# Kernel optimization log

Hardware: AMD Instinct MI355X
Metric: run time of the kernel (lower is better)

Reference implementation:

```python
import jax, jax.numpy as jnp
import numpy as np

N = 50000      # nodes
E = 800000     # edges (avg degree 16)
F_IN = 512
HID = 128
OUT = 40


def setup_inputs() -> dict:
    key = jax.random.key(0)
    ks = jax.random.split(key, 6)
    x = jax.random.normal(ks[0], (N, F_IN), dtype=jnp.float32)
    edge_index = jax.random.randint(ks[1], (2, E), 0, N, dtype=jnp.int64)
    edge_weight = jax.random.uniform(ks[2], (E,), dtype=jnp.float32)
    # Glorot-ish init for the two GCNConv weight matrices
    W1 = jax.random.normal(ks[3], (F_IN, HID), dtype=jnp.float32) * (1.0 / np.sqrt(F_IN))
    b1 = jnp.zeros((HID,), dtype=jnp.float32)
    W2 = jax.random.normal(ks[4], (HID, OUT), dtype=jnp.float32) * (1.0 / np.sqrt(HID))
    b2 = jnp.zeros((OUT,), dtype=jnp.float32)
    return {"x": x, "edge_index": edge_index, "edge_weight": edge_weight,
            "W1": W1, "b1": b1, "W2": W2, "b2": b2}


def gcn_layer(x, edge_index, edge_weight, W, b):
    """PyG GCNConv (normalize=True, add_self_loops=True):
    out = D^{-1/2} (A + I) D^{-1/2} (x @ W) + b, with weighted edges."""
    n = x.shape[0]
    h = x @ W  # [n, F_out] dense transform before aggregation
    sl = jnp.arange(n)
    row = jnp.concatenate([edge_index[0], sl])   # source nodes
    col = jnp.concatenate([edge_index[1], sl])   # target nodes
    w = jnp.concatenate([edge_weight, jnp.ones((n,), x.dtype)])  # self-loop weight 1
    deg = jax.ops.segment_sum(w, col, num_segments=n)            # in-degree (weighted)
    dinv = jnp.where(deg > 0, jax.lax.rsqrt(deg), 0.0)
    norm = dinv[row] * w * dinv[col]                             # per-edge coefficient
    # gather-source, scale, scatter-add into target
    out = jax.ops.segment_sum(h[row] * norm[:, None], col, num_segments=n)
    return out + b


def reference(x, edge_index, edge_weight, W1, b1, W2, b2):
    h = jax.nn.relu(gcn_layer(x, edge_index, edge_weight, W1, b1))
    # dropout is identity at inference (training=False)
    h = gcn_layer(h, edge_index, edge_weight, W2, b2)
    return jax.nn.log_softmax(h, axis=1)
```

## Files before the change

### kernel.cpp

```cpp
#include <hip/hip_runtime.h>
#include <math.h>

#define N_NODES 50000
#define F_IN    512
#define HID     128
#define OUT_C   40
#define NPAD    48
#define E_EDGES 800000
#define SCAN_BLOCKS 196
#define LDA 40
#define LDK 136
#define MAXDEG 96
#define G1B 391
#define DEGB 3125

typedef __attribute__((ext_vector_type(8))) short short8;
typedef __attribute__((ext_vector_type(4))) float f32x4;

__device__ __forceinline__ unsigned short f2bf(float f) {
    union { float f; unsigned u; } v; v.f = f;
    unsigned u = v.u + 0x7fffu + ((v.u >> 16) & 1u);
    return (unsigned short)(u >> 16);
}
__device__ __forceinline__ float bf2f(unsigned short h) {
    return __uint_as_float((unsigned)h << 16);
}


__global__ void k_init(unsigned long long* __restrict__ packed) {
    int i = blockIdx.x * blockDim.x + threadIdx.x;
    if (i < N_NODES) packed[i] = 0ULL;
}


__global__ __launch_bounds__(256) void k_wprep(const float* __restrict__ W1,
                                               const float* __restrict__ W2,
                                               unsigned short* __restrict__ W1bt,
                                               unsigned short* __restrict__ W2bt) {
    int idx = blockIdx.x * 256 + threadIdx.x;
    if (idx < F_IN * HID) {
        int k = idx & 511, n = idx >> 9;
        W1bt[(size_t)n * F_IN + k] = f2bf(W1[(size_t)k * HID + n]);
    } else if (idx < F_IN * HID + NPAD * HID) {
        int i2 = idx - F_IN * HID;
        int k = i2 & 127, n = i2 >> 7;
        W2bt[n * HID + k] = (n < OUT_C) ? f2bf(W2[(size_t)k * OUT_C + n]) : 0;
    }
}


__global__ __launch_bounds__(256) void k_g1deg(const float* __restrict__ X,
                                               const unsigned short* __restrict__ W1bt,
                                               unsigned short* __restrict__ Hb,
                                               const int* __restrict__ col,
                                               const float* __restrict__ ew,
                                               unsigned long long* __restrict__ packed,
                                               int* __restrict__ rank) {
    const int tid = threadIdx.x;
    if (blockIdx.x >= G1B) {
        int e = (blockIdx.x - G1B) * 256 + tid;
        if (e < E_EDGES) {
            int c = col[e];
            unsigned long long fx = (unsigned long long)(ew[e] * 4294967296.0f);
            unsigned long long old = atomicAdd(&packed[c], (1ULL << 40) | fx);
            rank[e] = (int)(old >> 40);
        }
        return;
    }

    __shared__ __align__(16) unsigned short As[128 * LDA];
    __shared__ __align__(16) unsigned short Bs[128 * LDA];
    const int row0 = blockIdx.x * 128;
    const int lane = tid & 63;
    const int w    = tid >> 6;
    const int quad = lane >> 4;
    const int l16  = lane & 15;
    const int wm   = (w >> 1) * 64;
    const int wn   = (w & 1) * 64;

    f32x4 acc[4][4] = {};

    const int sr = tid >> 1;
    const int kg = (tid & 1) * 16;
    int arow = row0 + sr;
    if (arow >= N_NODES) arow = N_NODES - 1;
    const float*          xp = X + (size_t)arow * F_IN + kg;
    const unsigned short* bp = W1bt + (size_t)sr * F_IN + kg;
    unsigned short* asw = &As[sr * LDA + kg];
    unsigned short* bsw = &Bs[sr * LDA + kg];

    for (int k0 = 0; k0 < F_IN; k0 += 32) {
        float4 xa = *(const float4*)(xp + k0);
        float4 xb = *(const float4*)(xp + k0 + 4);
        float4 xc = *(const float4*)(xp + k0 + 8);
        float4 xd = *(const float4*)(xp + k0 + 12);
        short8 pa, pb;
        pa[0] = (short)f2bf(xa.x); pa[1] = (short)f2bf(xa.y);
        pa[2] = (short)f2bf(xa.z); pa[3] = (short)f2bf(xa.w);
        pa[4] = (short)f2bf(xb.x); pa[5] = (short)f2bf(xb.y);
        pa[6] = (short)f2bf(xb.z); pa[7] = (short)f2bf(xb.w);
        pb[0] = (short)f2bf(xc.x); pb[1] = (short)f2bf(xc.y);
        pb[2] = (short)f2bf(xc.z); pb[3] = (short)f2bf(xc.w);
        pb[4] = (short)f2bf(xd.x); pb[5] = (short)f2bf(xd.y);
        pb[6] = (short)f2bf(xd.z); pb[7] = (short)f2bf(xd.w);
        short8 wa = *(const short8*)(bp + k0);
        short8 wb = *(const short8*)(bp + k0 + 8);

        *(short8*)(asw)     = pa;
        *(short8*)(asw + 8) = pb;
        *(short8*)(bsw)     = wa;
        *(short8*)(bsw + 8) = wb;
        __syncthreads();

        short8 af[4], bf[4];
#pragma unroll
        for (int i = 0; i < 4; i++)
            af[i] = *(const short8*)&As[(wm + i * 16 + l16) * LDA + quad * 8];
#pragma unroll
        for (int j = 0; j < 4; j++)
            bf[j] = *(const short8*)&Bs[(wn + j * 16 + l16) * LDA + quad * 8];
#pragma unroll
        for (int i = 0; i < 4; i++)
#pragma unroll
            for (int j = 0; j < 4; j++)
                acc[i][j] = __builtin_amdgcn_mfma_f32_16x16x32_bf16(
                    af[i], bf[j], acc[i][j], 0, 0, 0);
        __syncthreads();
    }

#pragma unroll
    for (int i = 0; i < 4; i++) {
#pragma unroll
        for (int r = 0; r < 4; r++) {
            int grow = row0 + wm + i * 16 + quad * 4 + r;
            if (grow < N_NODES) {
#pragma unroll
                for (int j = 0; j < 4; j++) {
                    int gcol = wn + j * 16 + l16;
                    Hb[(size_t)grow * HID + gcol] = f2bf(acc[i][j][r]);
                }
            }
        }
    }
}


__global__ __launch_bounds__(256) void k_scan1(const unsigned long long* __restrict__ packed,
                                               int* __restrict__ excl,
                                               int* __restrict__ bsum,
                                               float* __restrict__ dinv) {
    __shared__ int s[256];
    int tid = threadIdx.x;
    int i = blockIdx.x * 256 + tid;
    unsigned long long pk = (i < N_NODES) ? packed[i] : 0ULL;
    int v = (int)(pk >> 40);
    if (i < N_NODES) {
        float d = 1.0f + (float)(pk & 0xFFFFFFFFFFULL) * (1.0f / 4294967296.0f);
        dinv[i] = rsqrtf(d);
    }
    s[tid] = v;
    __syncthreads();
#pragma unroll
    for (int off = 1; off < 256; off <<= 1) {
        int t = (tid >= off) ? s[tid - off] : 0;
        __syncthreads();
        s[tid] += t;
        __syncthreads();
    }
    if (i < N_NODES) excl[i] = s[tid] - v;
    if (tid == 255) bsum[blockIdx.x] = s[255];
}

__global__ __launch_bounds__(256) void k_scan2(int* __restrict__ bsum) {
    __shared__ int s[256];
    int tid = threadIdx.x;
    int v = (tid < SCAN_BLOCKS) ? bsum[tid] : 0;
    s[tid] = v;
    __syncthreads();
#pragma unroll
    for (int off = 1; off < 256; off <<= 1) {
        int t = (tid >= off) ? s[tid - off] : 0;
        __syncthreads();
        s[tid] += t;
        __syncthreads();
    }
    if (tid < SCAN_BLOCKS) bsum[tid] = s[tid] - v;
}

__global__ __launch_bounds__(256) void k_scan3(int* __restrict__ rowptr,
                                               const int* __restrict__ bsum) {
    int i = blockIdx.x * 256 + threadIdx.x;
    if (i < N_NODES) rowptr[i] += bsum[blockIdx.x];
    if (i == 0) rowptr[N_NODES] = E_EDGES;
}


__global__ void k_scatter(const int* __restrict__ row, const int* __restrict__ col,
                          const float* __restrict__ w, const float* __restrict__ dinv,
                          const int* __restrict__ rowptr, const int* __restrict__ rank,
                          int2* __restrict__ es) {
    int e = blockIdx.x * blockDim.x + threadIdx.x;
    if (e < E_EDGES) {
        int r = row[e], c = col[e];
        float pre = dinv[r] * w[e];
        int pos = rowptr[c] + rank[e];
        es[pos] = make_int2(r, __float_as_int(pre));
    }
}


__global__ __launch_bounds__(256) void k_agg1_csr(const int* __restrict__ rowptr,
                                                  const int2* __restrict__ es,
                                                  const float* __restrict__ dinv,
                                                  const unsigned short* __restrict__ H1b,
                                                  const float* __restrict__ b1,
                                                  unsigned short* __restrict__ A1b) {
    __shared__ int2 sE[4][MAXDEG];
    const int tid  = threadIdx.x;
    const int wv   = tid >> 6;
    const int lane = tid & 63;
    const int node = blockIdx.x * 4 + wv;
    if (node >= N_NODES) return;

    const int beg = rowptr[node];
    const int d   = rowptr[node + 1] - beg;
    const int dl  = (d < MAXDEG) ? d : MAXDEG;
    const int dp  = (dl + 7) & ~7;
    for (int p = lane; p < dp; p += 64)
        sE[wv][p] = (p < dl) ? es[beg + p] : make_int2(0, 0);

    const float di = dinv[node];
    const unsigned self = *(const unsigned*)&H1b[(size_t)node * HID + lane * 2];
    float al0 = di * __uint_as_float(self << 16);
    float ah0 = di * __uint_as_float(self & 0xffff0000u);
    float al1 = 0.0f, ah1 = 0.0f, al2 = 0.0f, ah2 = 0.0f, al3 = 0.0f, ah3 = 0.0f;

    for (int p = 0; p < dp; p += 8) {
        int s[8]; float n[8]; unsigned g[8];
#pragma unroll
        for (int j = 0; j < 8; j++) {
            int2 t = sE[wv][p + j];
            s[j] = t.x; n[j] = __int_as_float(t.y);
        }
#pragma unroll
        for (int j = 0; j < 8; j++)
            g[j] = *(const unsigned*)&H1b[(size_t)s[j] * HID + lane * 2];
        al0 = fmaf(__uint_as_float(g[0] << 16), n[0], al0);
        ah0 = fmaf(__uint_as_float(g[0] & 0xffff0000u), n[0], ah0);
        al1 = fmaf(__uint_as_float(g[1] << 16), n[1], al1);
        ah1 = fmaf(__uint_as_float(g[1] & 0xffff0000u), n[1], ah1);
        al2 = fmaf(__uint_as_float(g[2] << 16), n[2], al2);
        ah2 = fmaf(__uint_as_float(g[2] & 0xffff0000u), n[2], ah2);
        al3 = fmaf(__uint_as_float(g[3] << 16), n[3], al3);
        ah3 = fmaf(__uint_as_float(g[3] & 0xffff0000u), n[3], ah3);
        al0 = fmaf(__uint_as_float(g[4] << 16), n[4], al0);
        ah0 = fmaf(__uint_as_float(g[4] & 0xffff0000u), n[4], ah0);
        al1 = fmaf(__uint_as_float(g[5] << 16), n[5], al1);
        ah1 = fmaf(__uint_as_float(g[5] & 0xffff0000u), n[5], ah1);
        al2 = fmaf(__uint_as_float(g[6] << 16), n[6], al2);
        ah2 = fmaf(__uint_as_float(g[6] & 0xffff0000u), n[6], ah2);
        al3 = fmaf(__uint_as_float(g[7] << 16), n[7], al3);
        ah3 = fmaf(__uint_as_float(g[7] & 0xffff0000u), n[7], ah3);
    }
    for (int q = dl; q < d; ++q) {
        int2 t = es[beg + q];
        unsigned g = *(const unsigned*)&H1b[(size_t)t.x * HID + lane * 2];
        float nm = __int_as_float(t.y);
        al0 = fmaf(__uint_as_float(g << 16), nm, al0);
        ah0 = fmaf(__uint_as_float(g & 0xffff0000u), nm, ah0);
    }

    const float accl = (al0 + al1) + (al2 + al3);
    const float acch = (ah0 + ah1) + (ah2 + ah3);
    const int c = lane * 2;
    float rx = fmaxf(fmaf(di, accl, b1[c]), 0.0f);
    float ry = fmaxf(fmaf(di, acch, b1[c + 1]), 0.0f);
    unsigned pack = (unsigned)f2bf(rx) | ((unsigned)f2bf(ry) << 16);
    *(unsigned*)&A1b[(size_t)node * HID + c] = pack;
}


__global__ __launch_bounds__(256) void k_gemm2_mfma(const unsigned short* __restrict__ A1b,
                                                    const unsigned short* __restrict__ W2bt,
                                                    unsigned short* __restrict__ H2b) {
    __shared__ __align__(16) unsigned short As[128 * LDK];
    __shared__ __align__(16) unsigned short Bs[NPAD * LDK];
    const int tid  = threadIdx.x;
    const int row0 = blockIdx.x * 128;
    const int lane = tid & 63;
    const int w    = tid >> 6;
    const int quad = lane >> 4;
    const int l16  = lane & 15;

#pragma unroll
    for (int i = 0; i < 8; i++) {
        int id = tid + i * 256;
        int r = id >> 4, kc = (id & 15) * 8;
        int ar = row0 + r; if (ar >= N_NODES) ar = N_NODES - 1;
        *(short8*)&As[r * LDK + kc] = *(const short8*)&A1b[(size_t)ar * HID + kc];
    }
#pragma unroll
    for (int i = 0; i < 3; i++) {
        int id = tid + i * 256;
        int n = id >> 4, kc = (id & 15) * 8;
        *(short8*)&Bs[n * LDK + kc] = *(const short8*)&W2bt[n * HID + kc];
    }
    __syncthreads();

    f32x4 acc[2][3] = {};
    const int rbase = w * 32;
#pragma unroll
    for (int ks = 0; ks < 4; ks++) {
        const int k0 = ks * 32 + quad * 8;
        short8 af[2], bf[3];
#pragma unroll
        for (int i = 0; i < 2; i++)
            af[i] = *(const short8*)&As[(rbase + i * 16 + l16) * LDK + k0];
#pragma unroll
        for (int j = 0; j < 3; j++)
            bf[j] = *(const short8*)&Bs[(j * 16 + l16) * LDK + k0];
#pragma unroll
        for (int i = 0; i < 2; i++)
#pragma unroll
            for (int j = 0; j < 3; j++)
                acc[i][j] = __builtin_amdgcn_mfma_f32_16x16x32_bf16(
                    af[i], bf[j], acc[i][j], 0, 0, 0);
    }

#pragma unroll
    for (int i = 0; i < 2; i++) {
#pragma unroll
        for (int r = 0; r < 4; r++) {
            int grow = row0 + rbase + i * 16 + quad * 4 + r;
            if (grow < N_NODES) {
#pragma unroll
                for (int j = 0; j < 3; j++)
                    H2b[(size_t)grow * NPAD + j * 16 + l16] = f2bf(acc[i][j][r]);
            }
        }
    }
}


__global__ __launch_bounds__(256) void k_agg2_lsm(const int* __restrict__ rowptr,
                                                  const int2* __restrict__ es,
                                                  const float* __restrict__ dinv,
                                                  const unsigned short* __restrict__ H2b,
                                                  const float* __restrict__ b2,
                                                  float* __restrict__ out) {
    __shared__ int2 sE[4][MAXDEG];
    const int tid  = threadIdx.x;
    const int wv   = tid >> 6;
    const int lane = tid & 63;
    const int node = blockIdx.x * 4 + wv;
    if (node >= N_NODES) return;

    const int beg = rowptr[node];
    const int d   = rowptr[node + 1] - beg;
    const int dl = (d < MAXDEG) ? d : MAXDEG;
    const int dp = (dl + 7) & ~7;
    for (int p = lane; p < dp; p += 64)
        sE[wv][p] = (p < dl) ? es[beg + p] : make_int2(0, 0);

    float di = dinv[node];
    float a0 = 0.0f, a1 = 0.0f, a2 = 0.0f, a3 = 0.0f;
    if (lane < OUT_C) a0 = di * bf2f(H2b[(size_t)node * NPAD + lane]);

    for (int p = 0; p < dp; p += 8) {
        int s[8]; float n[8], v[8];
#pragma unroll
        for (int j = 0; j < 8; j++) {
            int2 t = sE[wv][p + j];
            s[j] = t.x; n[j] = __int_as_float(t.y);
        }
#pragma unroll
        for (int j = 0; j < 8; j++)
            v[j] = (lane < OUT_C) ? bf2f(H2b[(size_t)s[j] * NPAD + lane]) : 0.0f;
        a0 = fmaf(v[0], n[0], a0);  a1 = fmaf(v[1], n[1], a1);
        a2 = fmaf(v[2], n[2], a2);  a3 = fmaf(v[3], n[3], a3);
        a0 = fmaf(v[4], n[4], a0);  a1 = fmaf(v[5], n[5], a1);
        a2 = fmaf(v[6], n[6], a2);  a3 = fmaf(v[7], n[7], a3);
    }
    for (int q = dl; q < d; ++q)
        if (lane < OUT_C) {
            int2 t = es[beg + q];
            a0 = fmaf(bf2f(H2b[(size_t)t.x * NPAD + lane]), __int_as_float(t.y), a0);
        }

    float acc = (a0 + a1) + (a2 + a3);
    float v = (lane < OUT_C) ? fmaf(di, acc, b2[lane]) : -INFINITY;

    float m = v;
#pragma unroll
    for (int off = 32; off > 0; off >>= 1) m = fmaxf(m, __shfl_xor(m, off));
    float ex = (lane < OUT_C) ? __expf(v - m) : 0.0f;
    float s = ex;
#pragma unroll
    for (int off = 32; off > 0; off >>= 1) s += __shfl_xor(s, off);
    if (lane < OUT_C) out[(size_t)node * OUT_C + lane] = v - m - __logf(s);
}


extern "C" void kernel_launch(void* const* d_in, const int* in_sizes, int n_in,
                              void* d_out, int out_size, void* d_ws, size_t ws_size,
                              hipStream_t stream) {
    const float* x  = (const float*)d_in[0];
    const int*   ei = (const int*)d_in[1];
    const float* ew = (const float*)d_in[2];
    const float* W1 = (const float*)d_in[3];
    const float* b1 = (const float*)d_in[4];
    const float* W2 = (const float*)d_in[5];
    const float* b2 = (const float*)d_in[6];
    float* out = (float*)d_out;

    const int* row = ei;
    const int* col = ei + E_EDGES;

    float* ws = (float*)d_ws;
    unsigned long long* packed = (unsigned long long*)ws;
    float* dinv   = ws + 100000;
    int*   rowptr = (int*)(ws + 150000);
    int*   bsum   = (int*)(ws + 200016);
    int2*  es     = (int2*)(ws + 200272);
    int*   rank   = (int*)(ws + 1800272);
    unsigned short* H1b  = (unsigned short*)(ws + 2600272);
    unsigned short* A1b  = (unsigned short*)(ws + 5800272);
    unsigned short* W1bt = (unsigned short*)(ws + 9000272);
    unsigned short* W2bt = (unsigned short*)(ws + 9033040);
    unsigned short* H2b  = (unsigned short*)(ws + 9036112);

    const int B = 256;

    k_init<<<(N_NODES + B - 1) / B, B, 0, stream>>>(packed);
    k_wprep<<<(F_IN * HID + NPAD * HID + B - 1) / B, B, 0, stream>>>(W1, W2, W1bt, W2bt);

    k_g1deg<<<G1B + DEGB, B, 0, stream>>>(x, W1bt, H1b, col, ew, packed, rank);

    k_scan1<<<SCAN_BLOCKS, B, 0, stream>>>(packed, rowptr, bsum, dinv);
    k_scan2<<<1, B, 0, stream>>>(bsum);
    k_scan3<<<SCAN_BLOCKS, B, 0, stream>>>(rowptr, bsum);

    k_scatter<<<(E_EDGES + B - 1) / B, B, 0, stream>>>(row, col, ew, dinv,
                                                       rowptr, rank, es);

    k_agg1_csr<<<(N_NODES + 3) / 4, B, 0, stream>>>(rowptr, es, dinv, H1b, b1, A1b);

    k_gemm2_mfma<<<(N_NODES + 127) / 128, B, 0, stream>>>(A1b, W2bt, H2b);

    k_agg2_lsm<<<(N_NODES + 3) / 4, B, 0, stream>>>(rowptr, es, dinv, H2b, b2, out);
}
```

Baseline: 310.0 us.

## Replace global-atomic degree counting with LDS chunked histograms for CSR build

Degree and rank computation moves from 64-bit global atomics per edge to per-block LDS histograms over 32 edge chunks × 4 node ranges. The per-chunk partial counts are scanned into absolute per-chunk offsets. A new scatter kernel recomputes local ranks with LDS atomics, so the rank array and the init kernel are no longer needed. Edge weights are now summed as 10-bit fixed point, which reduces degree precision. Only 128 blocks handle the histogram and scatter work, each rereading col, and the scans now read and write a 6.4MB partial array.

```diff
diff --git a/kernel.cpp b/kernel.cpp
--- a/kernel.cpp
+++ b/kernel.cpp
@@ -12,7 +12,10 @@
 #define LDK 136
 #define MAXDEG 96
 #define G1B 391
-#define DEGB 3125
+#define NCHUNK 32
+#define NRANGE 4
+#define RNODES 12500
+#define CHUNK_E 25000
 
 typedef __attribute__((ext_vector_type(8))) short short8;
 typedef __attribute__((ext_vector_type(4))) float f32x4;
@@ -24,12 +27,6 @@
 }
 __device__ __forceinline__ float bf2f(unsigned short h) {
     return __uint_as_float((unsigned)h << 16);
-}
-
-
-__global__ void k_init(unsigned long long* __restrict__ packed) {
-    int i = blockIdx.x * blockDim.x + threadIdx.x;
-    if (i < N_NODES) packed[i] = 0ULL;
 }
 
 
@@ -49,27 +46,39 @@
 }
 
 
-__global__ __launch_bounds__(256) void k_g1deg(const float* __restrict__ X,
-                                               const unsigned short* __restrict__ W1bt,
-                                               unsigned short* __restrict__ Hb,
-                                               const int* __restrict__ col,
-                                               const float* __restrict__ ew,
-                                               unsigned long long* __restrict__ packed,
-                                               int* __restrict__ rank) {
+__global__ __launch_bounds__(256) void k_g1hist(const float* __restrict__ X,
+                                                const unsigned short* __restrict__ W1bt,
+                                                unsigned short* __restrict__ Hb,
+                                                const int* __restrict__ col,
+                                                const float* __restrict__ ew,
+                                                unsigned* __restrict__ partial) {
+    __shared__ __align__(16) unsigned smem[12544];
     const int tid = threadIdx.x;
+
     if (blockIdx.x >= G1B) {
-        int e = (blockIdx.x - G1B) * 256 + tid;
-        if (e < E_EDGES) {
-            int c = col[e];
-            unsigned long long fx = (unsigned long long)(ew[e] * 4294967296.0f);
-            unsigned long long old = atomicAdd(&packed[c], (1ULL << 40) | fx);
-            rank[e] = (int)(old >> 40);
-        }
+        const int hb = blockIdx.x - G1B;
+        const int nc = hb >> 2, nr = hb & 3;
+        const int nbase = nr * RNODES;
+        unsigned* cnt = smem;
+        for (int i = tid; i < RNODES; i += 256) cnt[i] = 0u;
+        __syncthreads();
+        const int e0 = nc * CHUNK_E;
+        for (int k = tid; k < CHUNK_E; k += 256) {
+            int e = e0 + k;
+            unsigned cr = (unsigned)(col[e] - nbase);
+            if (cr < (unsigned)RNODES) {
+                unsigned fx = (unsigned)(ew[e] * 1024.0f + 0.5f);
+                atomicAdd(&cnt[cr], (1u << 16) | fx);
+            }
+        }
+        __syncthreads();
+        for (int i = tid; i < RNODES; i += 256)
+            partial[(size_t)nc * N_NODES + nbase + i] = cnt[i];
         return;
     }
 
-    __shared__ __align__(16) unsigned short As[128 * LDA];
-    __shared__ __align__(16) unsigned short Bs[128 * LDA];
+    unsigned short* As = (unsigned short*)smem;
+    unsigned short* Bs = As + 128 * LDA;
     const int row0 = blockIdx.x * 128;
     const int lane = tid & 63;
     const int w    = tid >> 6;
@@ -145,18 +154,26 @@
 }
 
 
-__global__ __launch_bounds__(256) void k_scan1(const unsigned long long* __restrict__ packed,
+__global__ __launch_bounds__(256) void k_scan1(unsigned* __restrict__ partial,
                                                int* __restrict__ excl,
                                                int* __restrict__ bsum,
                                                float* __restrict__ dinv) {
     __shared__ int s[256];
     int tid = threadIdx.x;
     int i = blockIdx.x * 256 + tid;
-    unsigned long long pk = (i < N_NODES) ? packed[i] : 0ULL;
-    int v = (int)(pk >> 40);
+    int v = 0;
     if (i < N_NODES) {
-        float d = 1.0f + (float)(pk & 0xFFFFFFFFFFULL) * (1.0f / 4294967296.0f);
-        dinv[i] = rsqrtf(d);
+        unsigned ctot = 0; float wsum = 0.0f;
+#pragma unroll
+        for (int nc = 0; nc < NCHUNK; nc++) {
+            size_t idx = (size_t)nc * N_NODES + i;
+            unsigned p = partial[idx];
+            partial[idx] = ctot;
+            ctot += p >> 16;
+            wsum += (float)(p & 0xffffu);
+        }
+        dinv[i] = rsqrtf(1.0f + wsum * (1.0f / 1024.0f));
+        v = (int)ctot;
     }
     s[tid] = v;
     __syncthreads();
@@ -187,24 +204,46 @@
     if (tid < SCAN_BLOCKS) bsum[tid] = s[tid] - v;
 }
 
+
 __global__ __launch_bounds__(256) void k_scan3(int* __restrict__ rowptr,
-                                               const int* __restrict__ bsum) {
+                                               const int* __restrict__ bsum,
+                                               unsigned* __restrict__ partial) {
     int i = blockIdx.x * 256 + threadIdx.x;
-    if (i < N_NODES) rowptr[i] += bsum[blockIdx.x];
+    if (i < N_NODES) {
+        int rp = rowptr[i] + bsum[blockIdx.x];
+        rowptr[i] = rp;
+#pragma unroll
+        for (int nc = 0; nc < NCHUNK; nc++)
+            partial[(size_t)nc * N_NODES + i] += (unsigned)rp;
+    }
     if (i == 0) rowptr[N_NODES] = E_EDGES;
 }
 
 
-__global__ void k_scatter(const int* __restrict__ row, const int* __restrict__ col,
-                          const float* __restrict__ w, const float* __restrict__ dinv,
-                          const int* __restrict__ rowptr, const int* __restrict__ rank,
-                          int2* __restrict__ es) {
-    int e = blockIdx.x * blockDim.x + threadIdx.x;
-    if (e < E_EDGES) {
-        int r = row[e], c = col[e];
-        float pre = dinv[r] * w[e];
-        int pos = rowptr[c] + rank[e];
-        es[pos] = make_int2(r, __float_as_int(pre));
+__global__ __launch_bounds__(256) void k_scatter2(const int* __restrict__ row,
+                                                  const int* __restrict__ col,
+                                                  const float* __restrict__ ew,
+                                                  const float* __restrict__ dinv,
+                                                  const unsigned* __restrict__ cbabs,
+                                                  int2* __restrict__ es) {
+    __shared__ unsigned cnt[RNODES];
+    const int tid = threadIdx.x;
+    const int nc = blockIdx.x >> 2, nr = blockIdx.x & 3;
+    const int nbase = nr * RNODES;
+    for (int i = tid; i < RNODES; i += 256) cnt[i] = 0u;
+    __syncthreads();
+    const int e0 = nc * CHUNK_E;
+    for (int k = tid; k < CHUNK_E; k += 256) {
+        int e = e0 + k;
+        int c = col[e];
+        unsigned cr = (unsigned)(c - nbase);
+        if (cr < (unsigned)RNODES) {
+            unsigned local = atomicAdd(&cnt[cr], 1u);
+            unsigned pos = cbabs[(size_t)nc * N_NODES + c] + local;
+            int r = row[e];
+            float pre = dinv[r] * ew[e];
+            es[pos] = make_int2(r, __float_as_int(pre));
+        }
     }
 }
 
@@ -417,31 +456,28 @@
     const int* col = ei + E_EDGES;
 
     float* ws = (float*)d_ws;
-    unsigned long long* packed = (unsigned long long*)ws;
-    float* dinv   = ws + 100000;
-    int*   rowptr = (int*)(ws + 150000);
-    int*   bsum   = (int*)(ws + 200016);
-    int2*  es     = (int2*)(ws + 200272);
-    int*   rank   = (int*)(ws + 1800272);
-    unsigned short* H1b  = (unsigned short*)(ws + 2600272);
-    unsigned short* A1b  = (unsigned short*)(ws + 5800272);
-    unsigned short* W1bt = (unsigned short*)(ws + 9000272);
-    unsigned short* W2bt = (unsigned short*)(ws + 9033040);
-    unsigned short* H2b  = (unsigned short*)(ws + 9036112);
+    unsigned* partial = (unsigned*)ws;
+    float* dinv   = ws + 1600000;
+    int*   rowptr = (int*)(ws + 1650016);
+    int*   bsum   = (int*)(ws + 1700032);
+    int2*  es     = (int2*)(ws + 1700352);
+    unsigned short* H1b  = (unsigned short*)(ws + 3300352);
+    unsigned short* A1b  = (unsigned short*)(ws + 6500352);
+    unsigned short* W1bt = (unsigned short*)(ws + 9700352);
+    unsigned short* W2bt = (unsigned short*)(ws + 9733120);
+    unsigned short* H2b  = (unsigned short*)(ws + 9736192);
 
     const int B = 256;
 
-    k_init<<<(N_NODES + B - 1) / B, B, 0, stream>>>(packed);
     k_wprep<<<(F_IN * HID + NPAD * HID + B - 1) / B, B, 0, stream>>>(W1, W2, W1bt, W2bt);
 
-    k_g1deg<<<G1B + DEGB, B, 0, stream>>>(x, W1bt, H1b, col, ew, packed, rank);
-
-    k_scan1<<<SCAN_BLOCKS, B, 0, stream>>>(packed, rowptr, bsum, dinv);
+    k_g1hist<<<G1B + NCHUNK * NRANGE, B, 0, stream>>>(x, W1bt, H1b, col, ew, partial);
+
+    k_scan1<<<SCAN_BLOCKS, B, 0, stream>>>(partial, rowptr, bsum, dinv);
     k_scan2<<<1, B, 0, stream>>>(bsum);
-    k_scan3<<<SCAN_BLOCKS, B, 0, stream>>>(rowptr, bsum);
-
-    k_scatter<<<(E_EDGES + B - 1) / B, B, 0, stream>>>(row, col, ew, dinv,
-                                                       rowptr, rank, es);
+    k_scan3<<<SCAN_BLOCKS, B, 0, stream>>>(rowptr, bsum, partial);
+
+    k_scatter2<<<NCHUNK * NRANGE, B, 0, stream>>>(row, col, ew, dinv, partial, es);
 
     k_agg1_csr<<<(N_NODES + 3) / 4, B, 0, stream>>>(rowptr, es, dinv, H1b, b1, A1b);
 
```

After: 428.4 us. 1.38x slower.

## Fuse init into wprep, merge scan stages, batch edges per thread, nontemporal loads

Applied to the files above, without the earlier changes.

Zeroing of the packed degree array moves into the weight-prep kernel, and the single-block scan2 is folded into scan3, where every block redundantly rescans the block sums. Together these remove two kernel launches. The degree-counting and scatter kernels now handle four edges per thread with fewer blocks, issuing the atomics before storing ranks. Nontemporal loads are used for X in the GEMM and for the edge arrays. The aim is less launch overhead and better memory-level parallelism, at the cost of redundant scan work in every block.

```diff
diff --git a/kernel.cpp b/kernel.cpp
--- a/kernel.cpp
+++ b/kernel.cpp
@@ -12,7 +12,8 @@
 #define LDK 136
 #define MAXDEG 96
 #define G1B 391
-#define DEGB 3125
+#define DEGB 782
+#define SCATB 782
 
 typedef __attribute__((ext_vector_type(8))) short short8;
 typedef __attribute__((ext_vector_type(4))) float f32x4;
@@ -27,16 +28,11 @@
 }
 
 
-__global__ void k_init(unsigned long long* __restrict__ packed) {
-    int i = blockIdx.x * blockDim.x + threadIdx.x;
-    if (i < N_NODES) packed[i] = 0ULL;
-}
-
-
 __global__ __launch_bounds__(256) void k_wprep(const float* __restrict__ W1,
                                                const float* __restrict__ W2,
                                                unsigned short* __restrict__ W1bt,
-                                               unsigned short* __restrict__ W2bt) {
+                                               unsigned short* __restrict__ W2bt,
+                                               unsigned long long* __restrict__ packed) {
     int idx = blockIdx.x * 256 + threadIdx.x;
     if (idx < F_IN * HID) {
         int k = idx & 511, n = idx >> 9;
@@ -45,6 +41,9 @@
         int i2 = idx - F_IN * HID;
         int k = i2 & 127, n = i2 >> 7;
         W2bt[n * HID + k] = (n < OUT_C) ? f2bf(W2[(size_t)k * OUT_C + n]) : 0;
+    } else {
+        int i3 = idx - (F_IN * HID + NPAD * HID);
+        if (i3 < N_NODES) packed[i3] = 0ULL;
     }
 }
 
@@ -58,12 +57,22 @@
                                                int* __restrict__ rank) {
     const int tid = threadIdx.x;
     if (blockIdx.x >= G1B) {
-        int e = (blockIdx.x - G1B) * 256 + tid;
-        if (e < E_EDGES) {
-            int c = col[e];
-            unsigned long long fx = (unsigned long long)(ew[e] * 4294967296.0f);
-            unsigned long long old = atomicAdd(&packed[c], (1ULL << 40) | fx);
-            rank[e] = (int)(old >> 40);
+        const int e0 = (blockIdx.x - G1B) * 1024 + tid;
+        unsigned long long old[4];
+#pragma unroll
+        for (int j = 0; j < 4; j++) {
+            int e = e0 + j * 256;
+            if (e < E_EDGES) {
+                int c = __builtin_nontemporal_load(col + e);
+                float w = __builtin_nontemporal_load(ew + e);
+                unsigned long long fx = (unsigned long long)(w * 4294967296.0f);
+                old[j] = atomicAdd(&packed[c], (1ULL << 40) | fx);
+            }
+        }
+#pragma unroll
+        for (int j = 0; j < 4; j++) {
+            int e = e0 + j * 256;
+            if (e < E_EDGES) rank[e] = (int)(old[j] >> 40);
         }
         return;
     }
@@ -90,10 +99,10 @@
     unsigned short* bsw = &Bs[sr * LDA + kg];
 
     for (int k0 = 0; k0 < F_IN; k0 += 32) {
-        float4 xa = *(const float4*)(xp + k0);
-        float4 xb = *(const float4*)(xp + k0 + 4);
-        float4 xc = *(const float4*)(xp + k0 + 8);
-        float4 xd = *(const float4*)(xp + k0 + 12);
+        f32x4 xa = __builtin_nontemporal_load((const f32x4*)(xp + k0));
+        f32x4 xb = __builtin_nontemporal_load((const f32x4*)(xp + k0 + 4));
+        f32x4 xc = __builtin_nontemporal_load((const f32x4*)(xp + k0 + 8));
+        f32x4 xd = __builtin_nontemporal_load((const f32x4*)(xp + k0 + 12));
         short8 pa, pb;
         pa[0] = (short)f2bf(xa.x); pa[1] = (short)f2bf(xa.y);
         pa[2] = (short)f2bf(xa.z); pa[3] = (short)f2bf(xa.w);
@@ -171,7 +180,9 @@
     if (tid == 255) bsum[blockIdx.x] = s[255];
 }
 
-__global__ __launch_bounds__(256) void k_scan2(int* __restrict__ bsum) {
+
+__global__ __launch_bounds__(256) void k_scan3(int* __restrict__ rowptr,
+                                               const int* __restrict__ bsum) {
     __shared__ int s[256];
     int tid = threadIdx.x;
     int v = (tid < SCAN_BLOCKS) ? bsum[tid] : 0;
@@ -184,27 +195,30 @@
         s[tid] += t;
         __syncthreads();
     }
-    if (tid < SCAN_BLOCKS) bsum[tid] = s[tid] - v;
-}
-
-__global__ __launch_bounds__(256) void k_scan3(int* __restrict__ rowptr,
-                                               const int* __restrict__ bsum) {
-    int i = blockIdx.x * 256 + threadIdx.x;
-    if (i < N_NODES) rowptr[i] += bsum[blockIdx.x];
+    int base = s[blockIdx.x] - ((blockIdx.x < SCAN_BLOCKS) ? bsum[blockIdx.x] : 0);
+    int i = blockIdx.x * 256 + tid;
+    if (i < N_NODES) rowptr[i] += base;
     if (i == 0) rowptr[N_NODES] = E_EDGES;
 }
 
 
-__global__ void k_scatter(const int* __restrict__ row, const int* __restrict__ col,
-                          const float* __restrict__ w, const float* __restrict__ dinv,
-                          const int* __restrict__ rowptr, const int* __restrict__ rank,
-                          int2* __restrict__ es) {
-    int e = blockIdx.x * blockDim.x + threadIdx.x;
-    if (e < E_EDGES) {
-        int r = row[e], c = col[e];
-        float pre = dinv[r] * w[e];
-        int pos = rowptr[c] + rank[e];
-        es[pos] = make_int2(r, __float_as_int(pre));
+__global__ __launch_bounds__(256) void k_scatter(const int* __restrict__ row,
+                                                 const int* __restrict__ col,
+                                                 const float* __restrict__ ew,
+                                                 const float* __restrict__ dinv,
+                                                 const int* __restrict__ rowptr,
+                                                 const int* __restrict__ rank,
+                                                 int2* __restrict__ es) {
+    const int e0 = blockIdx.x * 1024 + threadIdx.x;
+#pragma unroll
+    for (int j = 0; j < 4; j++) {
+        int e = e0 + j * 256;
+        if (e < E_EDGES) {
+            int r = row[e], c = col[e];
+            float pre = dinv[r] * ew[e];
+            int pos = rowptr[c] + rank[e];
+            es[pos] = make_int2(r, __float_as_int(pre));
+        }
     }
 }
 
@@ -431,17 +445,15 @@
 
     const int B = 256;
 
-    k_init<<<(N_NODES + B - 1) / B, B, 0, stream>>>(packed);
-    k_wprep<<<(F_IN * HID + NPAD * HID + B - 1) / B, B, 0, stream>>>(W1, W2, W1bt, W2bt);
+    k_wprep<<<(F_IN * HID + NPAD * HID + N_NODES + B - 1) / B, B, 0, stream>>>(
+        W1, W2, W1bt, W2bt, packed);
 
     k_g1deg<<<G1B + DEGB, B, 0, stream>>>(x, W1bt, H1b, col, ew, packed, rank);
 
     k_scan1<<<SCAN_BLOCKS, B, 0, stream>>>(packed, rowptr, bsum, dinv);
-    k_scan2<<<1, B, 0, stream>>>(bsum);
     k_scan3<<<SCAN_BLOCKS, B, 0, stream>>>(rowptr, bsum);
 
-    k_scatter<<<(E_EDGES + B - 1) / B, B, 0, stream>>>(row, col, ew, dinv,
-                                                       rowptr, rank, es);
+    k_scatter<<<SCATB, B, 0, stream>>>(row, col, ew, dinv, rowptr, rank, es);
 
     k_agg1_csr<<<(N_NODES + 3) / 4, B, 0, stream>>>(rowptr, es, dinv, H1b, b1, A1b);
 
```

Result: slower. 333.8 us (+7.7%).
